# Kernel optimization log

Hardware: AMD Instinct MI355X
Metric: run time of the kernel (lower is better)

## Reference

```python
import jax, jax.numpy as jnp
import numpy as np

# Dims: T time steps (PoissonEncoder seq_length=50), batch B, input N_IN, hidden H, labels L
T, B, N_IN, H, L = 50, 1024, 784, 256, 10
DT = 0.001            # norse default dt
TAU_SYN_INV = 100.0   # 1/0.01
TAU_MEM_INV = 50.0    # 1/0.02
V_LEAK, V_TH, V_RESET = 0.0, 0.5, 0.0
ALPHA = 100.0         # SuperSpike surrogate slope

@jax.custom_vjp
def superspike(x):
    # Heaviside forward, SuperSpike surrogate backward (norse 'super' method)
    return (x > 0).astype(x.dtype)

def _ss_fwd(x):
    return superspike(x), x

def _ss_bwd(x, g):
    return (g / (ALPHA * jnp.abs(x) + 1.0) ** 2,)

superspike.defvjp(_ss_fwd, _ss_bwd)

def setup_inputs() -> dict:
    key = jax.random.key(0)
    ks = jax.random.split(key, 5)
    # Poisson-encoded spike train, time-major [T, B, N_IN]
    x = (jax.random.uniform(ks[0], (T, B, N_IN)) < 0.3).astype(jnp.float32)
    Wi = jax.random.normal(ks[1], (H, N_IN), dtype=jnp.float32) / np.float32(np.sqrt(N_IN))
    Wr = jax.random.normal(ks[2], (H, H), dtype=jnp.float32) / np.float32(np.sqrt(H))
    Wout = jax.random.normal(ks[3], (L, H), dtype=jnp.float32) / np.float32(np.sqrt(H))
    bout = jnp.zeros((L,), dtype=jnp.float32)
    return {"x": x, "Wi": Wi, "Wr": Wr, "Wout": Wout, "bout": bout}

def reference(x, Wi, Wr, Wout, bout):
    Tw, Bb, _ = x.shape
    Hh = Wi.shape[0]
    Ll = Wout.shape[0]
    z0 = jnp.zeros((Bb, Hh), x.dtype)
    acc0 = jnp.zeros((Bb, Ll), x.dtype)

    def step(carry, x_t):
        z, v, i, acc = carry
        # LIF dynamics (norse lif_step)
        v_dec = v + DT * TAU_MEM_INV * ((V_LEAK - v) + i)   # voltage integration
        i_dec = i * (1.0 - DT * TAU_SYN_INV)                # synaptic current decay
        z_new = superspike(v_dec - V_TH)                    # spike
        v_new = (1.0 - z_new) * v_dec + z_new * V_RESET     # reset
        i_new = i_dec + x_t @ Wi.T + z @ Wr.T               # input + recurrent drive
        # per-step readout accumulation
        acc = acc + z_new @ Wout.T + bout
        return (z_new, v_new, i_new, acc), None

    (_, _, _, acc), _ = jax.lax.scan(step, (z0, z0, z0, acc0), x)
    return acc / Tw  # outputs.float() / time_window (is_test=False path)
```

## Files before the change

kernel.cpp:

```cpp
#include <hip/hip_runtime.h>
#include <cstdint>
#include <cstddef>

#define T_STEPS 50
#define B_SZ    1024
#define N_INP   784
#define H_SZ    256
#define L_SZ    10
#define M_TOT   (T_STEPS * B_SZ)
#define NK0     26
#define NSLICE  5

typedef int v4i  __attribute__((ext_vector_type(4)));
typedef int v16i __attribute__((ext_vector_type(16)));

__global__ __launch_bounds__(256) void transpose_wr(const float* __restrict__ Wr,
                                                    float* __restrict__ WrTz) {
    __shared__ float tile[32][33];
    int bx = blockIdx.x * 32, by = blockIdx.y * 32;
    int tx = threadIdx.x % 32, ty = threadIdx.x / 32;
    #pragma unroll
    for (int j = 0; j < 32; j += 8)
        tile[ty + j][tx] = Wr[(size_t)(by + ty + j) * H_SZ + bx + tx];
    if (blockIdx.x == 0 && blockIdx.y == 0)
        WrTz[(size_t)256 * H_SZ + threadIdx.x] = 0.0f;
    __syncthreads();
    #pragma unroll
    for (int j = 0; j < 32; j += 8)
        WrTz[(size_t)(bx + ty + j) * H_SZ + by + tx] = tile[tx][ty + j];
}

__global__ __launch_bounds__(128) void prep_packed(const float* __restrict__ Wi,
                                                   uint8_t* __restrict__ SBp) {
    const int nt   = blockIdx.x;
    const int k0   = blockIdx.y * 2 + (threadIdx.x >> 6);
    const int lane = threadIdx.x & 63;
    const int h    = nt * 32 + (lane & 31);
    const int g    = k0 * 2 + (lane >> 5);

    int wd[NSLICE][4] = {};
    #pragma unroll
    for (int u = 0; u < 16; ++u) {
        double wv = 0.0;
        if (g < 49) wv = (double)Wi[(size_t)h * N_INP + g * 16 + u];
        double r = rint(wv * 0x1p40);
        #pragma unroll
        for (int j = 0; j < NSLICE - 1; ++j) {
            double q  = floor((r + 128.0) * 0.00390625);
            double dj = r - 256.0 * q;
            wd[j][u >> 2] |= ((int)dj & 0xFF) << ((u & 3) * 8);
            r = q;
        }
        wd[NSLICE - 1][u >> 2] |= ((int)r & 0xFF) << ((u & 3) * 8);
    }
    uint8_t* base = SBp + ((size_t)(nt * NK0 + k0) * NSLICE) * 1024 + lane * 16;
    #pragma unroll
    for (int j = 0; j < NSLICE; ++j)
        *(v4i*)(base + (size_t)j * 1024) = (v4i){wd[j][0], wd[j][1], wd[j][2], wd[j][3]};
}

__global__ __launch_bounds__(256) void pack_x(const float* __restrict__ X,
                                              uint8_t* __restrict__ Ap) {
    const int mt  = blockIdx.x;
    const int tid = threadIdx.x;
    #pragma unroll
    for (int i = 0; i < 7; ++i) {
        int s = tid + i * 256;
        if (s < NK0 * 64) {
            int k0 = s >> 6, lane = s & 63;
            int m = mt * 32 + (lane & 31);
            int g = k0 * 2 + (lane >> 5);
            unsigned int bw[4] = {0u, 0u, 0u, 0u};
            if (g < 49) {
                const float* src = X + (size_t)m * N_INP + g * 16;
                #pragma unroll
                for (int q = 0; q < 4; ++q) {
                    float4 f = *(const float4*)(src + q * 4);
                    bw[q] = (f.x != 0.f ? 1u : 0u) | (f.y != 0.f ? 0x100u : 0u)
                          | (f.z != 0.f ? 0x10000u : 0u) | (f.w != 0.f ? 0x1000000u : 0u);
                }
            }
            *(v4i*)(Ap + ((size_t)(mt * NK0 + k0)) * 1024 + lane * 16) =
                (v4i){(int)bw[0], (int)bw[1], (int)bw[2], (int)bw[3]};
        }
    }
}

__global__ __launch_bounds__(256) void gemm_i8s(const uint8_t* __restrict__ Ap,
                                                const uint8_t* __restrict__ SBp,
                                                double* __restrict__ cur) {
    __shared__ __align__(16) uint8_t Bs[2][2 * NSLICE * 1024];

    const int tid   = threadIdx.x;
    const int wave  = tid >> 6;
    const int lane  = tid & 63;
    const int ghalf = lane >> 5;
    const int nt    = blockIdx.y;
    const int mt0   = (blockIdx.x * 4 + wave) * 2;
    const int mt1   = mt0 + 1;

    const uint8_t* ap0 = Ap + (size_t)mt0 * NK0 * 1024 + lane * 16;
    const uint8_t* ap1 = Ap + (size_t)mt1 * NK0 * 1024 + lane * 16;
    const uint8_t* bbase = SBp + ((size_t)nt * NK0 * NSLICE) * 1024;

    {
        const uint8_t* src = bbase;
        #pragma unroll
        for (int i = 0; i < 2; ++i) {
            int s = tid + i * 256;
            *(v4i*)(Bs[0] + s * 16) = *(const v4i*)(src + s * 16);
        }
        if (tid < 128) {
            int s = tid + 512;
            *(v4i*)(Bs[0] + s * 16) = *(const v4i*)(src + s * 16);
        }
    }
    v4i a0c = *(const v4i*)(ap0);
    v4i a0n = *(const v4i*)(ap0 + 1024);
    v4i a1c = *(const v4i*)(ap1);
    v4i a1n = *(const v4i*)(ap1 + 1024);
    __syncthreads();

    v16i acc0[NSLICE] = {};
    v16i acc1[NSLICE] = {};

    for (int p = 0; p < 13; ++p) {
        const int cb = p & 1;
        v4i b0c = a0c, b0n = a0n, b1c = a1c, b1n = a1n;
        if (p < 12) {
            const uint8_t* src = bbase + (size_t)(p + 1) * 2 * NSLICE * 1024;
            uint8_t* dst = Bs[cb ^ 1];
            #pragma unroll
            for (int i = 0; i < 2; ++i) {
                int s = tid + i * 256;
                *(v4i*)(dst + s * 16) = *(const v4i*)(src + s * 16);
            }
            if (tid < 128) {
                int s = tid + 512;
                *(v4i*)(dst + s * 16) = *(const v4i*)(src + s * 16);
            }
            a0c = *(const v4i*)(ap0 + (size_t)(2 * p + 2) * 1024);
            a0n = *(const v4i*)(ap0 + (size_t)(2 * p + 3) * 1024);
            a1c = *(const v4i*)(ap1 + (size_t)(2 * p + 2) * 1024);
            a1n = *(const v4i*)(ap1 + (size_t)(2 * p + 3) * 1024);
        }
        #pragma unroll
        for (int dk = 0; dk < 2; ++dk) {
            v4i aa0 = dk ? b0n : b0c;
            v4i aa1 = dk ? b1n : b1c;
            #pragma unroll
            for (int j = 0; j < NSLICE; ++j) {
                v4i b = *(const v4i*)(Bs[cb] + (dk * NSLICE + j) * 1024 + lane * 16);
                acc0[j] = __builtin_amdgcn_mfma_i32_32x32x32_i8(aa0, b, acc0[j], 0, 0, 0);
                acc1[j] = __builtin_amdgcn_mfma_i32_32x32x32_i8(aa1, b, acc1[j], 0, 0, 0);
            }
        }
        __syncthreads();
    }

    const int h = nt * 32 + (lane & 31);
    #pragma unroll
    for (int r = 0; r < 16; ++r) {
        int mloc = (r & 3) + 8 * (r >> 2) + 4 * ghalf;
        double s0 = (double)acc0[4][r];
        s0 = s0 * 256.0 + (double)acc0[3][r];
        s0 = s0 * 256.0 + (double)acc0[2][r];
        s0 = s0 * 256.0 + (double)acc0[1][r];
        s0 = s0 * 256.0 + (double)acc0[0][r];
        cur[(size_t)(mt0 * 32 + mloc) * H_SZ + h] = s0 * 0x1p-40;
        double s1 = (double)acc1[4][r];
        s1 = s1 * 256.0 + (double)acc1[3][r];
        s1 = s1 * 256.0 + (double)acc1[2][r];
        s1 = s1 * 256.0 + (double)acc1[1][r];
        s1 = s1 * 256.0 + (double)acc1[0][r];
        cur[(size_t)(mt1 * 32 + mloc) * H_SZ + h] = s1 * 0x1p-40;
    }
}

#define SNN_STEP(T_CUR, P_, Q_, nnLp, nnGp, nnLq, nnGq)                           \
  {                                                                               \
                                          \
    double v_dec = v + 0.05 * ((0.0 - v) + syn);                                  \
    double i_dec = 0.9 * syn;                                                     \
    bool   z_new = v_dec > 0.5;                                                   \
    v = z_new ? 0.0 : v_dec;                                                      \
    cnt += z_new ? 1 : 0;                                                         \
    unsigned long long bal = __ballot((int)z_new);                                \
    if (lane == 0) zmS[Q_][bl][wv] = bal;                                         \
    __syncthreads();                               \
          \
    int tn = ((T_CUR) < T_STEPS - 1) ? (T_CUR) + 1 : (T_CUR);                     \
    double inp_n = curb[(size_t)tn * (B_SZ * H_SZ)];                              \
                      \
    {                                                                             \
      unsigned long long m0 = zmS[Q_][bl][0], m1 = zmS[Q_][bl][1],                \
                         m2 = zmS[Q_][bl][2], m3 = zmS[Q_][bl][3];                \
      int c0 = __popcll(m0), c1 = __popcll(m1);                                   \
      int c2 = __popcll(m2), c3 = __popcll(m3);                                   \
      int cL = c0 + c1, cG = c2 + c3;                                             \
      unsigned long long word = (h < 64) ? m0 : (h < 128) ? m1                    \
                               : (h < 192) ? m2 : m3;                             \
      int bit = h & 63;                                                           \
      bool act = (word >> bit) & 1ull;                                            \
      int pos = __popcll(word & ((1ull << bit) - 1ull));                          \
      if (h < 128) {                                                              \
        if (act) listL[Q_][bl][((h >> 6) ? c0 : 0) + pos] = h << 8;               \
        if (h < 16) listL[Q_][bl][cL + h] = 128 << 8;           \
      } else {                                                                    \
        if (act) listG[Q_][bl][(((h >> 6) == 3) ? c2 : 0) + pos] = h << 10;       \
        if (h < 144) listG[Q_][bl][cG + (h - 128)] = 256 << 10;    \
      }                                                                           \
      nnLq = cL; nnGq = cG;                                                       \
    }                                                                             \
        \
    double r0 = 0.0, r1 = 0.0, r2 = 0.0, r3 = 0.0;                                \
    const int nG = nnGp, nL = nnLp;                                               \
    const int* lg = &listG[P_][bl][0];                                            \
    const int* ll = &listL[P_][bl][0];                                            \
    float g0, g1, g2, g3, g4, g5, g6, g7;                                         \
    if (nG > 0) {                                        \
      v4i w0 = *(const v4i*)(lg);                                                 \
      v4i w1 = *(const v4i*)(lg + 4);                                             \
      g0 = *(const float*)(wrb + ((uint32_t)w0.x + hoff));                        \
      g1 = *(const float*)(wrb + ((uint32_t)w0.y + hoff));                        \
      g2 = *(const float*)(wrb + ((uint32_t)w0.z + hoff));                        \
      g3 = *(const float*)(wrb + ((uint32_t)w0.w + hoff));                        \
      g4 = *(const float*)(wrb + ((uint32_t)w1.x + hoff));                        \
      g5 = *(const float*)(wrb + ((uint32_t)w1.y + hoff));                        \
      g6 = *(const float*)(wrb + ((uint32_t)w1.z + hoff));                        \
      g7 = *(const float*)(wrb + ((uint32_t)w1.w + hoff));                        \
    }                                                                             \
    for (int j = 0; j < nL; j += 8) {                             \
      v4i u0 = *(const v4i*)(ll + j);                                             \
      v4i u1 = *(const v4i*)(ll + j + 4);                                         \
      float e0 = wrlh[u0.x], e1 = wrlh[u0.y], e2 = wrlh[u0.z], e3 = wrlh[u0.w];   \
      float e4 = wrlh[u1.x], e5 = wrlh[u1.y], e6 = wrlh[u1.z], e7 = wrlh[u1.w];   \
      r0 += (double)e0 + (double)e1;                                              \
      r1 += (double)e2 + (double)e3;                                              \
      r2 += (double)e4 + (double)e5;                                              \
      r3 += (double)e6 + (double)e7;                                              \
    }                                                                             \
    for (int j = 0; j < nG; j += 8) {               \
      float c0f = g0, c1f = g1, c2f = g2, c3f = g3;                               \
      float c4f = g4, c5f = g5, c6f = g6, c7f = g7;                               \
      v4i w0 = *(const v4i*)(lg + j + 8);                \
      v4i w1 = *(const v4i*)(lg + j + 12);                                        \
      g0 = *(const float*)(wrb + ((uint32_t)w0.x + hoff));                        \
      g1 = *(const float*)(wrb + ((uint32_t)w0.y + hoff));                        \
      g2 = *(const float*)(wrb + ((uint32_t)w0.z + hoff));                        \
      g3 = *(const float*)(wrb + ((uint32_t)w0.w + hoff));                        \
      g4 = *(const float*)(wrb + ((uint32_t)w1.x + hoff));                        \
      g5 = *(const float*)(wrb + ((uint32_t)w1.y + hoff));                        \
      g6 = *(const float*)(wrb + ((uint32_t)w1.z + hoff));                        \
      g7 = *(const float*)(wrb + ((uint32_t)w1.w + hoff));                        \
      r0 += (double)c0f + (double)c1f;                                            \
      r1 += (double)c2f + (double)c3f;                                            \
      r2 += (double)c4f + (double)c5f;                                            \
      r3 += (double)c6f + (double)c7f;                                            \
    }                                                                             \
    syn = (i_dec + inp_c) + ((r0 + r1) + (r2 + r3));                              \
    inp_c = inp_n;                                                                \
  }

__global__ __launch_bounds__(1024) void snn_scan(const double* __restrict__ cur,
                                                 const float* __restrict__ WrTz,
                                                 const float* __restrict__ Wout,
                                                 const float* __restrict__ bout,
                                                 float* __restrict__ out) {
    const int tid  = threadIdx.x;
    const int bl   = tid >> 8;
    const int h    = tid & 255;
    const int lane = tid & 63;
    const int wv   = (tid >> 6) & 3;
    const int b    = blockIdx.x * 4 + bl;

    __shared__ __align__(16) float WrL[129 * 256];
    __shared__ unsigned long long zmS[2][4][4];
    __shared__ __align__(16) int listL[2][4][144];
    __shared__ __align__(16) int listG[2][4][144];
    __shared__ float cntS[4][256];

    for (int s = tid; s < (129 * 256) / 4; s += 1024) {
        float4 val = (s < 8192) ? ((const float4*)WrTz)[s]
                                : make_float4(0.f, 0.f, 0.f, 0.f);
        ((float4*)WrL)[s] = val;
    }
    __syncthreads();

    double v = 0.0, syn = 0.0;
    int cnt = 0;
    int nnL0 = 0, nnG0 = 0, nnL1 = 0, nnG1 = 0;

    const double*  curb = cur + (size_t)b * H_SZ + h;
    const char*    wrb  = (const char*)WrTz;
    const float*   wrlh = WrL + h;
    const uint32_t hoff = (uint32_t)(h * 4);
    double inp_c = curb[0];

    for (int t2 = 0; t2 < T_STEPS; t2 += 2) {
        SNN_STEP(t2,     0, 1, nnL0, nnG0, nnL1, nnG1);
        SNN_STEP(t2 + 1, 1, 0, nnL1, nnG1, nnL0, nnG0);
    }

    cntS[bl][h] = (float)cnt;
    __syncthreads();
    if (h < L_SZ) {
        double s = 0.0;
        for (int k = 0; k < H_SZ; ++k)
            s += (double)cntS[bl][k] * (double)Wout[(size_t)h * H_SZ + k];
        s += (double)T_STEPS * (double)bout[h];
        out[(size_t)b * L_SZ + h] = (float)(s / (double)T_STEPS);
    }
}

extern "C" void kernel_launch(void* const* d_in, const int* in_sizes, int n_in,
                              void* d_out, int out_size, void* d_ws, size_t ws_size,
                              hipStream_t stream) {
    const float* x    = (const float*)d_in[0];
    const float* Wi   = (const float*)d_in[1];
    const float* Wr   = (const float*)d_in[2];
    const float* Wout = (const float*)d_in[3];
    const float* bout = (const float*)d_in[4];
    float* out = (float*)d_out;

    char* ws = (char*)d_ws;
    double*  cur  = (double*)(ws);
    float*   WrTz = (float*)(ws + 104857600);
    uint8_t* SBp  = (uint8_t*)(ws + 105121792);
    uint8_t* Ap   = (uint8_t*)(ws + 106186752);

    hipLaunchKernelGGL(transpose_wr, dim3(8, 8), dim3(256), 0, stream, Wr, WrTz);
    hipLaunchKernelGGL(prep_packed, dim3(8, 13), dim3(128), 0, stream, Wi, SBp);
    hipLaunchKernelGGL(pack_x, dim3(M_TOT / 32), dim3(256), 0, stream, x, Ap);
    hipLaunchKernelGGL(gemm_i8s, dim3(M_TOT / 256, 8), dim3(256), 0, stream, Ap, SBp, cur);
    hipLaunchKernelGGL(snn_scan, dim3(B_SZ / 4), dim3(1024), 0, stream,
                       cur, WrTz, Wout, bout, out);
}
```

Measured before the change: 401.4 us.

## Replace per-step block barrier with per-batch LDS tag spin-waits in SNN scan

Removes the __syncthreads each time step and replaces it with volatile LDS tag counters, so only the four wavefronts sharing a batch row synchronise, through spin-waits with explicit lgkmcnt fences. The spike-list build is moved after the recurrent gather so the previous step's lists are consumed before being overwritten, and the gather loops are software-pipelined deeper (two-stage prefetch for global, one-stage for LDS), with padding lists enlarged to 32 entries. This aims to decouple the four batch groups in a block and hide gather latency, at the cost of spin-wait polling and fragile memory-ordering assumptions between wavefronts.

```diff
diff --git a/kernel.cpp b/kernel.cpp
--- a/kernel.cpp
+++ b/kernel.cpp
@@ -171,95 +171,155 @@
         double s1 = (double)acc1[4][r];
         s1 = s1 * 256.0 + (double)acc1[3][r];
         s1 = s1 * 256.0 + (double)acc1[2][r];
-        s1 = s1 * 256.0 + (double)acc1[1][r];
+        s1 = s1 * 256.0 + (double)acc1[0 + 1][r];
         s1 = s1 * 256.0 + (double)acc1[0][r];
         cur[(size_t)(mt1 * 32 + mloc) * H_SZ + h] = s1 * 0x1p-40;
     }
 }
 
-#define SNN_STEP(T_CUR, P_, Q_, nnLp, nnGp, nnLq, nnGq)                           \
-  {                                                                               \
-                                          \
-    double v_dec = v + 0.05 * ((0.0 - v) + syn);                                  \
-    double i_dec = 0.9 * syn;                                                     \
-    bool   z_new = v_dec > 0.5;                                                   \
-    v = z_new ? 0.0 : v_dec;                                                      \
-    cnt += z_new ? 1 : 0;                                                         \
-    unsigned long long bal = __ballot((int)z_new);                                \
-    if (lane == 0) zmS[Q_][bl][wv] = bal;                                         \
-    __syncthreads();                               \
-          \
-    int tn = ((T_CUR) < T_STEPS - 1) ? (T_CUR) + 1 : (T_CUR);                     \
-    double inp_n = curb[(size_t)tn * (B_SZ * H_SZ)];                              \
-                      \
-    {                                                                             \
-      unsigned long long m0 = zmS[Q_][bl][0], m1 = zmS[Q_][bl][1],                \
-                         m2 = zmS[Q_][bl][2], m3 = zmS[Q_][bl][3];                \
-      int c0 = __popcll(m0), c1 = __popcll(m1);                                   \
-      int c2 = __popcll(m2), c3 = __popcll(m3);                                   \
-      int cL = c0 + c1, cG = c2 + c3;                                             \
-      unsigned long long word = (h < 64) ? m0 : (h < 128) ? m1                    \
-                               : (h < 192) ? m2 : m3;                             \
-      int bit = h & 63;                                                           \
-      bool act = (word >> bit) & 1ull;                                            \
-      int pos = __popcll(word & ((1ull << bit) - 1ull));                          \
-      if (h < 128) {                                                              \
-        if (act) listL[Q_][bl][((h >> 6) ? c0 : 0) + pos] = h << 8;               \
-        if (h < 16) listL[Q_][bl][cL + h] = 128 << 8;           \
-      } else {                                                                    \
-        if (act) listG[Q_][bl][(((h >> 6) == 3) ? c2 : 0) + pos] = h << 10;       \
-        if (h < 144) listG[Q_][bl][cG + (h - 128)] = 256 << 10;    \
-      }                                                                           \
-      nnLq = cL; nnGq = cG;                                                       \
-    }                                                                             \
-        \
-    double r0 = 0.0, r1 = 0.0, r2 = 0.0, r3 = 0.0;                                \
-    const int nG = nnGp, nL = nnLp;                                               \
-    const int* lg = &listG[P_][bl][0];                                            \
-    const int* ll = &listL[P_][bl][0];                                            \
-    float g0, g1, g2, g3, g4, g5, g6, g7;                                         \
-    if (nG > 0) {                                        \
-      v4i w0 = *(const v4i*)(lg);                                                 \
-      v4i w1 = *(const v4i*)(lg + 4);                                             \
-      g0 = *(const float*)(wrb + ((uint32_t)w0.x + hoff));                        \
-      g1 = *(const float*)(wrb + ((uint32_t)w0.y + hoff));                        \
-      g2 = *(const float*)(wrb + ((uint32_t)w0.z + hoff));                        \
-      g3 = *(const float*)(wrb + ((uint32_t)w0.w + hoff));                        \
-      g4 = *(const float*)(wrb + ((uint32_t)w1.x + hoff));                        \
-      g5 = *(const float*)(wrb + ((uint32_t)w1.y + hoff));                        \
-      g6 = *(const float*)(wrb + ((uint32_t)w1.z + hoff));                        \
-      g7 = *(const float*)(wrb + ((uint32_t)w1.w + hoff));                        \
-    }                                                                             \
-    for (int j = 0; j < nL; j += 8) {                             \
-      v4i u0 = *(const v4i*)(ll + j);                                             \
-      v4i u1 = *(const v4i*)(ll + j + 4);                                         \
-      float e0 = wrlh[u0.x], e1 = wrlh[u0.y], e2 = wrlh[u0.z], e3 = wrlh[u0.w];   \
-      float e4 = wrlh[u1.x], e5 = wrlh[u1.y], e6 = wrlh[u1.z], e7 = wrlh[u1.w];   \
-      r0 += (double)e0 + (double)e1;                                              \
-      r1 += (double)e2 + (double)e3;                                              \
-      r2 += (double)e4 + (double)e5;                                              \
-      r3 += (double)e6 + (double)e7;                                              \
-    }                                                                             \
-    for (int j = 0; j < nG; j += 8) {               \
-      float c0f = g0, c1f = g1, c2f = g2, c3f = g3;                               \
-      float c4f = g4, c5f = g5, c6f = g6, c7f = g7;                               \
-      v4i w0 = *(const v4i*)(lg + j + 8);                \
-      v4i w1 = *(const v4i*)(lg + j + 12);                                        \
-      g0 = *(const float*)(wrb + ((uint32_t)w0.x + hoff));                        \
-      g1 = *(const float*)(wrb + ((uint32_t)w0.y + hoff));                        \
-      g2 = *(const float*)(wrb + ((uint32_t)w0.z + hoff));                        \
-      g3 = *(const float*)(wrb + ((uint32_t)w0.w + hoff));                        \
-      g4 = *(const float*)(wrb + ((uint32_t)w1.x + hoff));                        \
-      g5 = *(const float*)(wrb + ((uint32_t)w1.y + hoff));                        \
-      g6 = *(const float*)(wrb + ((uint32_t)w1.z + hoff));                        \
-      g7 = *(const float*)(wrb + ((uint32_t)w1.w + hoff));                        \
-      r0 += (double)c0f + (double)c1f;                                            \
-      r1 += (double)c2f + (double)c3f;                                            \
-      r2 += (double)c4f + (double)c5f;                                            \
-      r3 += (double)c6f + (double)c7f;                                            \
-    }                                                                             \
-    syn = (i_dec + inp_c) + ((r0 + r1) + (r2 + r3));                              \
-    inp_c = inp_n;                                                                \
+#define FENCE_LDS() asm volatile("s_waitcnt lgkmcnt(0)" ::: "memory")
+
+#define SNN_STEP(T_CUR, P_, Q_, nnLp, nnGp, nnLq, nnGq)                          \
+  {                                                                              \
+                                      \
+    double v_dec = v + 0.05 * ((0.0 - v) + syn);                                 \
+    double i_dec = 0.9 * syn;                                                    \
+    bool   z_new = v_dec > 0.5;                                                  \
+    v = z_new ? 0.0 : v_dec;                                                     \
+    cnt += z_new ? 1 : 0;                                                        \
+    unsigned long long bal = __ballot((int)z_new);                               \
+                                  \
+    if (lane == 0) zmS[P_][bl][wvg] = bal;                                       \
+    FENCE_LDS();                                                                 \
+    if (lane == 0) tagA[P_][bl][wvg] = (unsigned)(T_CUR) + 1u;                   \
+                  \
+    int tn = ((T_CUR) < T_STEPS - 1) ? (T_CUR) + 1 : (T_CUR);                    \
+    double inp_n = curb[(size_t)tn * (B_SZ * H_SZ)];                             \
+                                            \
+    while (tagB[Q_][bl][0] < (unsigned)(T_CUR) ||                                \
+           tagB[Q_][bl][1] < (unsigned)(T_CUR) ||                                \
+           tagB[Q_][bl][2] < (unsigned)(T_CUR) ||                                \
+           tagB[Q_][bl][3] < (unsigned)(T_CUR)) {}                               \
+    FENCE_LDS();                                                                 \
+                                                                  \
+    double r0 = 0.0, r1 = 0.0, r2 = 0.0, r3 = 0.0;                               \
+    {                                                                            \
+      const int nL = nnLp, nG = nnGp;                                            \
+      const int* ll = (const int*)&listL[Q_][bl][0];                             \
+      const int* lg = (const int*)&listG[Q_][bl][0];                             \
+                              \
+      float ga0, ga1, ga2, ga3, ga4, ga5, ga6, ga7;                              \
+      float gb0, gb1, gb2, gb3, gb4, gb5, gb6, gb7;                              \
+      {                                                                          \
+        v4i w0 = *(const v4i*)(lg);  v4i w1 = *(const v4i*)(lg + 4);             \
+        ga0 = *(const float*)(wrb + ((uint32_t)w0.x + hoff));                    \
+        ga1 = *(const float*)(wrb + ((uint32_t)w0.y + hoff));                    \
+        ga2 = *(const float*)(wrb + ((uint32_t)w0.z + hoff));                    \
+        ga3 = *(const float*)(wrb + ((uint32_t)w0.w + hoff));                    \
+        ga4 = *(const float*)(wrb + ((uint32_t)w1.x + hoff));                    \
+        ga5 = *(const float*)(wrb + ((uint32_t)w1.y + hoff));                    \
+        ga6 = *(const float*)(wrb + ((uint32_t)w1.z + hoff));                    \
+        ga7 = *(const float*)(wrb + ((uint32_t)w1.w + hoff));                    \
+        v4i y0 = *(const v4i*)(lg + 8); v4i y1 = *(const v4i*)(lg + 12);         \
+        gb0 = *(const float*)(wrb + ((uint32_t)y0.x + hoff));                    \
+        gb1 = *(const float*)(wrb + ((uint32_t)y0.y + hoff));                    \
+        gb2 = *(const float*)(wrb + ((uint32_t)y0.z + hoff));                    \
+        gb3 = *(const float*)(wrb + ((uint32_t)y0.w + hoff));                    \
+        gb4 = *(const float*)(wrb + ((uint32_t)y1.x + hoff));                    \
+        gb5 = *(const float*)(wrb + ((uint32_t)y1.y + hoff));                    \
+        gb6 = *(const float*)(wrb + ((uint32_t)y1.z + hoff));                    \
+        gb7 = *(const float*)(wrb + ((uint32_t)y1.w + hoff));                    \
+      }                                                                          \
+           \
+      float e0, e1, e2, e3, e4, e5, e6, e7;                                      \
+      {                                                                          \
+        v4i u0 = *(const v4i*)(ll); v4i u1 = *(const v4i*)(ll + 4);              \
+        e0 = wrlh[u0.x]; e1 = wrlh[u0.y]; e2 = wrlh[u0.z]; e3 = wrlh[u0.w];      \
+        e4 = wrlh[u1.x]; e5 = wrlh[u1.y]; e6 = wrlh[u1.z]; e7 = wrlh[u1.w];      \
+      }                                                                          \
+      for (int j = 0; j < nL; j += 8) {                                          \
+        float p0 = e0, p1 = e1, p2 = e2, p3 = e3;                                \
+        float p4 = e4, p5 = e5, p6 = e6, p7 = e7;                                \
+        v4i u0 = *(const v4i*)(ll + j + 8);                                      \
+        v4i u1 = *(const v4i*)(ll + j + 12);                                     \
+        e0 = wrlh[u0.x]; e1 = wrlh[u0.y]; e2 = wrlh[u0.z]; e3 = wrlh[u0.w];      \
+        e4 = wrlh[u1.x]; e5 = wrlh[u1.y]; e6 = wrlh[u1.z]; e7 = wrlh[u1.w];      \
+        r0 += (double)p0 + (double)p1;                                           \
+        r1 += (double)p2 + (double)p3;                                           \
+        r2 += (double)p4 + (double)p5;                                           \
+        r3 += (double)p6 + (double)p7;                                           \
+      }                                                                          \
+                                           \
+      for (int j = 0; j < nG; j += 16) {                                         \
+        float p0 = ga0, p1 = ga1, p2 = ga2, p3 = ga3;                            \
+        float p4 = ga4, p5 = ga5, p6 = ga6, p7 = ga7;                            \
+        {                                                                        \
+          v4i w0 = *(const v4i*)(lg + j + 16);                                   \
+          v4i w1 = *(const v4i*)(lg + j + 20);                                   \
+          ga0 = *(const float*)(wrb + ((uint32_t)w0.x + hoff));                  \
+          ga1 = *(const float*)(wrb + ((uint32_t)w0.y + hoff));                  \
+          ga2 = *(const float*)(wrb + ((uint32_t)w0.z + hoff));                  \
+          ga3 = *(const float*)(wrb + ((uint32_t)w0.w + hoff));                  \
+          ga4 = *(const float*)(wrb + ((uint32_t)w1.x + hoff));                  \
+          ga5 = *(const float*)(wrb + ((uint32_t)w1.y + hoff));                  \
+          ga6 = *(const float*)(wrb + ((uint32_t)w1.z + hoff));                  \
+          ga7 = *(const float*)(wrb + ((uint32_t)w1.w + hoff));                  \
+        }                                                                        \
+        r0 += (double)p0 + (double)p1;                                           \
+        r1 += (double)p2 + (double)p3;                                           \
+        r2 += (double)p4 + (double)p5;                                           \
+        r3 += (double)p6 + (double)p7;                                           \
+        float q0 = gb0, q1 = gb1, q2 = gb2, q3 = gb3;                            \
+        float q4 = gb4, q5 = gb5, q6 = gb6, q7 = gb7;                            \
+        {                                                                        \
+          v4i w0 = *(const v4i*)(lg + j + 24);                                   \
+          v4i w1 = *(const v4i*)(lg + j + 28);                                   \
+          gb0 = *(const float*)(wrb + ((uint32_t)w0.x + hoff));                  \
+          gb1 = *(const float*)(wrb + ((uint32_t)w0.y + hoff));                  \
+          gb2 = *(const float*)(wrb + ((uint32_t)w0.z + hoff));                  \
+          gb3 = *(const float*)(wrb + ((uint32_t)w0.w + hoff));                  \
+          gb4 = *(const float*)(wrb + ((uint32_t)w1.x + hoff));                  \
+          gb5 = *(const float*)(wrb + ((uint32_t)w1.y + hoff));                  \
+          gb6 = *(const float*)(wrb + ((uint32_t)w1.z + hoff));                  \
+          gb7 = *(const float*)(wrb + ((uint32_t)w1.w + hoff));                  \
+        }                                                                        \
+        r0 += (double)q0 + (double)q1;                                           \
+        r1 += (double)q2 + (double)q3;                                           \
+        r2 += (double)q4 + (double)q5;                                           \
+        r3 += (double)q6 + (double)q7;                                           \
+      }                                                                          \
+    }                                                                            \
+                           \
+    while (tagA[P_][bl][0] < (unsigned)(T_CUR) + 1u ||                           \
+           tagA[P_][bl][1] < (unsigned)(T_CUR) + 1u ||                           \
+           tagA[P_][bl][2] < (unsigned)(T_CUR) + 1u ||                           \
+           tagA[P_][bl][3] < (unsigned)(T_CUR) + 1u) {}                          \
+    FENCE_LDS();                                                                 \
+    {                                                                            \
+      unsigned long long m0 = zmS[P_][bl][0], m1 = zmS[P_][bl][1],               \
+                         m2 = zmS[P_][bl][2], m3 = zmS[P_][bl][3];               \
+      int c0 = __popcll(m0), c1 = __popcll(m1);                                  \
+      int c2 = __popcll(m2), c3 = __popcll(m3);                                  \
+      int cL = c0 + c1, cG = c2 + c3;                                            \
+      unsigned long long word = (h < 64) ? m0 : (h < 128) ? m1                   \
+                               : (h < 192) ? m2 : m3;                            \
+      int bit = h & 63;                                                          \
+      bool act = (word >> bit) & 1ull;                                           \
+      int pos = __popcll(word & ((1ull << bit) - 1ull));                         \
+      if (h < 128) {                                                             \
+        if (act) listL[P_][bl][((h >> 6) ? c0 : 0) + pos] = h << 8;              \
+        if (h < 32) listL[P_][bl][cL + h] = 128 << 8;          \
+      } else {                                                                   \
+        if (act) listG[P_][bl][(((h >> 6) == 3) ? c2 : 0) + pos] = h << 10;      \
+        if (h < 160) listG[P_][bl][cG + (h - 128)] = 256 << 10;   \
+      }                                                                          \
+      FENCE_LDS();                                                               \
+      if (lane == 0) tagB[P_][bl][wvg] = (unsigned)(T_CUR) + 1u;                 \
+      nnLq = cL; nnGq = cG;                                                      \
+    }                                                                            \
+                                                                          \
+    syn = (i_dec + inp_c) + ((r0 + r1) + (r2 + r3));                             \
+    inp_c = inp_n;                                                               \
   }
 
 __global__ __launch_bounds__(1024) void snn_scan(const double* __restrict__ cur,
@@ -270,20 +330,32 @@
     const int tid  = threadIdx.x;
     const int bl   = tid >> 8;
     const int h    = tid & 255;
+    const int wvg  = h >> 6;
     const int lane = tid & 63;
-    const int wv   = (tid >> 6) & 3;
     const int b    = blockIdx.x * 4 + bl;
 
     __shared__ __align__(16) float WrL[129 * 256];
-    __shared__ unsigned long long zmS[2][4][4];
-    __shared__ __align__(16) int listL[2][4][144];
-    __shared__ __align__(16) int listG[2][4][144];
+    __shared__ volatile unsigned long long zmS[2][4][4];
+    __shared__ volatile unsigned tagA[2][4][4];
+    __shared__ volatile unsigned tagB[2][4][4];
+    __shared__ __align__(16) int listL[2][4][160];
+    __shared__ __align__(16) int listG[2][4][160];
     __shared__ float cntS[4][256];
 
     for (int s = tid; s < (129 * 256) / 4; s += 1024) {
         float4 val = (s < 8192) ? ((const float4*)WrTz)[s]
                                 : make_float4(0.f, 0.f, 0.f, 0.f);
         ((float4*)WrL)[s] = val;
+    }
+    if (tid < 32) {
+        int pp = tid >> 4, gg = (tid >> 2) & 3, ww = tid & 3;
+        tagA[pp][gg][ww] = 0u;
+        tagB[pp][gg][ww] = 0u;
+        zmS[pp][gg][ww]  = 0ull;
+    }
+    if (h < 32) {
+        listL[0][bl][h] = 128 << 8;  listL[1][bl][h] = 128 << 8;
+        listG[0][bl][h] = 256 << 10; listG[1][bl][h] = 256 << 10;
     }
     __syncthreads();
 
@@ -298,8 +370,8 @@
     double inp_c = curb[0];
 
     for (int t2 = 0; t2 < T_STEPS; t2 += 2) {
-        SNN_STEP(t2,     0, 1, nnL0, nnG0, nnL1, nnG1);
-        SNN_STEP(t2 + 1, 1, 0, nnL1, nnG1, nnL0, nnG0);
+        SNN_STEP(t2,     0, 1, nnL1, nnG1, nnL0, nnG0);
+        SNN_STEP(t2 + 1, 1, 0, nnL0, nnG0, nnL1, nnG1);
     }
 
     cntS[bl][h] = (float)cnt;
```

After: 471.4 us. +17.4%, slower.
